# Performance work log

Measured on AMD Instinct MI355X. Metric: run time of the kernel, lower is better.

Reference implementation:

```python
import jax, jax.numpy as jnp
import numpy as np

B, N, D, H = 4, 2048, 1024, 16
HD = D // H
SCALE = D ** -0.5  # NOTE: original scales by dimension**-0.5 (not head_dim**-0.5)


def setup_inputs() -> dict:
    key = jax.random.key(0)
    k1, k2, k3 = jax.random.split(key, 3)
    x = jax.random.normal(k1, (B, N, D), dtype=jnp.float32)
    w_qkv = jax.random.normal(k2, (D, 3 * D), dtype=jnp.float32) * (D ** -0.5)
    w_proj = jax.random.normal(k3, (D, D), dtype=jnp.float32) * (D ** -0.5)
    b_proj = jnp.zeros((D,), dtype=jnp.float32)
    return {"x": x, "w_qkv": w_qkv, "w_proj": w_proj, "b_proj": b_proj}


def reference(x, w_qkv, w_proj, b_proj):
    # qkv projection: [B,N,3D] -> split into q,k,v each [B,H,N,HD]
    qkv = x @ w_qkv
    qkv = qkv.reshape(B, N, 3, H, HD).transpose(2, 0, 3, 1, 4)  # [3,B,H,N,HD]
    q, k, v = qkv[0], qkv[1], qkv[2]
    scores = jnp.einsum('bhid,bhjd->bhij', q, k) * SCALE
    attn = jax.nn.softmax(scores, axis=-1)
    out = jnp.einsum('bhij,bhjd->bhid', attn, v)  # [B,H,N,HD]
    out = out.transpose(0, 2, 1, 3).reshape(B, N, D)
    return out @ w_proj + b_proj
```

## Files before the change

kernel.cpp:

```cpp
#include <hip/hip_runtime.h>
#include <stdint.h>

#define Bdim 4
#define Nseq 2048
#define Dmod 1024
#define Hn   16
#define HD   64
#define SCALE 0.03125f
#define L2E   1.44269504089f

typedef __attribute__((ext_vector_type(8))) short short8;
typedef __attribute__((ext_vector_type(8))) unsigned short ushort8;
typedef __attribute__((ext_vector_type(4))) float f32x4;
typedef __attribute__((ext_vector_type(16))) float f32x16;

typedef __attribute__((address_space(3))) uint32_t lds_u32;
typedef __attribute__((address_space(1))) const uint32_t glob_u32;

static __device__ __forceinline__ void gload_lds16(const unsigned short* g, unsigned short* l) {
    __builtin_amdgcn_global_load_lds((glob_u32*)(const void*)g, (lds_u32*)(void*)l, 16, 0, 0);
}

static __device__ __forceinline__ unsigned short f2bf(float f) {
    union { float f; uint32_t u; } v; v.f = f;
    uint32_t r = (v.u + 0x7FFFu + ((v.u >> 16) & 1u)) >> 16;
    return (unsigned short)r;
}

__global__ __launch_bounds__(256) void cast_x_kernel(const float* __restrict__ in,
                                                     unsigned short* __restrict__ out, int n4) {
    int i = blockIdx.x * blockDim.x + threadIdx.x;
    int stride = gridDim.x * blockDim.x;
    for (; i < n4; i += stride) {
        float4 v = reinterpret_cast<const float4*>(in)[i];
        ushort4 o;
        o.x = f2bf(v.x); o.y = f2bf(v.y); o.z = f2bf(v.z); o.w = f2bf(v.w);
        reinterpret_cast<ushort4*>(out)[i] = o;
    }
}

__global__ void transpose_cast_kernel(const float* __restrict__ in,
                                      unsigned short* __restrict__ out, int R, int C) {
    __shared__ unsigned short t[32][33];
    int c0 = blockIdx.x * 32, r0 = blockIdx.y * 32;
    int tx = threadIdx.x, ty = threadIdx.y;
#pragma unroll
    for (int i = 0; i < 4; ++i)
        t[ty + i*8][tx] = f2bf(in[(size_t)(r0 + ty + i*8) * C + c0 + tx]);
    __syncthreads();
#pragma unroll
    for (int i = 0; i < 4; ++i)
        out[(size_t)(c0 + ty + i*8) * R + r0 + tx] = t[tx][ty + i*8];
}

template<bool OUT_BF16, bool BIAS>
__global__ __launch_bounds__(256) void gemm_bt_kernel(const unsigned short* __restrict__ A,
                                                      const unsigned short* __restrict__ Bt,
                                                      void* __restrict__ Cv,
                                                      const float* __restrict__ bias,
                                                      int M, int N, int K) {
    __shared__ unsigned short Al[128 * 64];
    __shared__ unsigned short Bl[128 * 64];
    int tid = threadIdx.x;
    int lane = tid & 63, wv = tid >> 6;
    int wr = (wv >> 1) * 64, wc = (wv & 1) * 64;
    int lr = lane & 15, lg = lane >> 4, lk = lg * 8;
    int m0 = blockIdx.y * 128, n0 = blockIdx.x * 128;

    int srow = wv * 8 + (lane >> 3);
    int scol = (lane & 7) * 8;
    const unsigned short* ag = A  + (size_t)(m0 + srow) * K + scol;
    const unsigned short* bg = Bt + (size_t)(n0 + srow) * K + scol;
    unsigned short* la = Al + wv * 512;
    unsigned short* lb = Bl + wv * 512;

    f32x4 acc[4][4];
#pragma unroll
    for (int i = 0; i < 4; ++i)
#pragma unroll
        for (int j = 0; j < 4; ++j) acc[i][j] = (f32x4)0.f;

    for (int k0 = 0; k0 < K; k0 += 64) {
        __syncthreads();
#pragma unroll
        for (int i = 0; i < 4; ++i) {
            gload_lds16(ag + (size_t)i * 32 * K + k0, la + i * 2048);
            gload_lds16(bg + (size_t)i * 32 * K + k0, lb + i * 2048);
        }
        __syncthreads();
#pragma unroll
        for (int ks = 0; ks < 2; ++ks) {
            short8 a[4], b[4];
#pragma unroll
            for (int mi = 0; mi < 4; ++mi)
                a[mi] = *reinterpret_cast<const short8*>(Al + (wr + mi*16 + lr) * 64 + ks*32 + lk);
#pragma unroll
            for (int nj = 0; nj < 4; ++nj)
                b[nj] = *reinterpret_cast<const short8*>(Bl + (wc + nj*16 + lr) * 64 + ks*32 + lk);
#pragma unroll
            for (int mi = 0; mi < 4; ++mi)
#pragma unroll
                for (int nj = 0; nj < 4; ++nj)
                    acc[mi][nj] = __builtin_amdgcn_mfma_f32_16x16x32_bf16(a[mi], b[nj], acc[mi][nj], 0, 0, 0);
        }
    }
#pragma unroll
    for (int mi = 0; mi < 4; ++mi) {
#pragma unroll
        for (int nj = 0; nj < 4; ++nj) {
            int r = m0 + wr + mi*16 + lg*4;
            int c = n0 + wc + nj*16 + lr;
            float bv = BIAS ? bias[c] : 0.f;
#pragma unroll
            for (int i = 0; i < 4; ++i) {
                float v = acc[mi][nj][i] + bv;
                if (OUT_BF16)
                    reinterpret_cast<unsigned short*>(Cv)[(size_t)(r + i) * N + c] = f2bf(v);
                else
                    reinterpret_cast<float*>(Cv)[(size_t)(r + i) * N + c] = v;
            }
        }
    }
}

__global__ __launch_bounds__(256) void transpose_v_kernel(const unsigned short* __restrict__ qkv,
                                                          unsigned short* __restrict__ vT) {
    __shared__ unsigned short t[64][68];
    int bh = blockIdx.y, b = bh >> 4, h = bh & 15;
    int j0 = blockIdx.x * 64;
    int tid = threadIdx.x;
#pragma unroll
    for (int p = 0; p < 4; ++p) {
        int e = p * 256 + tid;
        int jj = e >> 4;
        int d4 = (e & 15) * 4;
        const unsigned short* src = qkv + (size_t)(b*Nseq + j0 + jj) * 3072 + 2048 + h*64 + d4;
        ushort4 v = *reinterpret_cast<const ushort4*>(src);
        *reinterpret_cast<ushort4*>(&t[jj][d4]) = v;
    }
    __syncthreads();
#pragma unroll
    for (int p = 0; p < 4; ++p) {
        int e = p * 256 + tid;
        int d = e >> 4;
        int j4 = (e & 15) * 4;
        ushort4 v;
        v.x = t[j4 + 0][d]; v.y = t[j4 + 1][d]; v.z = t[j4 + 2][d]; v.w = t[j4 + 3][d];
        *reinterpret_cast<ushort4*>(vT + ((size_t)bh * 64 + d) * Nseq + j0 + j4) = v;
    }
}

__global__ __launch_bounds__(256, 2) void attn_kernel(const unsigned short* __restrict__ qkv,
                                                      const unsigned short* __restrict__ vT,
                                                      unsigned short* __restrict__ attn_o) {
    __shared__ unsigned short Kl[64 * 64];
    __shared__ unsigned short Vl[64 * 64];
    __shared__ unsigned short Pl[4 * 64 * 64];

    int w = blockIdx.x;
    int lid = (w & 7) * 64 + (w >> 3);
    int bh = lid >> 3, qb = lid & 7;
    int b = bh >> 4, h = bh & 15;

    int tid = threadIdx.x, lane = tid & 63, wv = tid >> 6;
    int lr = lane & 31, hi = lane >> 5;
    int q0 = qb * 256 + wv * 64;

    short8 qfA[4], qfB[4];
    {
        const unsigned short* qrowA = qkv + (size_t)(b * Nseq + q0 + lr) * 3072 + h * 64 + hi * 8;
        const unsigned short* qrowB = qrowA + (size_t)32 * 3072;
#pragma unroll
        for (int ks = 0; ks < 4; ++ks) {
            qfA[ks] = *reinterpret_cast<const short8*>(qrowA + ks * 16);
            qfB[ks] = *reinterpret_cast<const short8*>(qrowB + ks * 16);
        }
    }

    float mrunA = -1e30f, lrunA = 0.f, mrunB = -1e30f, lrunB = 0.f;
    f32x16 oA0 = (f32x16)0.f, oA1 = (f32x16)0.f, oB0 = (f32x16)0.f, oB1 = (f32x16)0.f;

    int sr = tid >> 2;
    int sc = (tid & 3) * 32;
    const unsigned short* kg = qkv + (size_t)(b * Nseq + sr) * 3072 + 1024 + h * 64 + sc / 2;
    const unsigned short* vg = vT + ((size_t)(bh * 64 + sr)) * Nseq + sc / 2;
    int swz0 = sr * 128 + ((sc) ^ ((sr & 7) << 4));
    int swz1 = sr * 128 + ((sc + 16) ^ ((sr & 7) << 4));
    int rswz = (lr & 7) << 4;
    char* PlW = (char*)Pl + wv * 8192 + lr * 128;

    ushort8 k0r = *reinterpret_cast<const ushort8*>(kg);
    ushort8 k1r = *reinterpret_cast<const ushort8*>(kg + 8);
    ushort8 v0r = *reinterpret_cast<const ushort8*>(vg);
    ushort8 v1r = *reinterpret_cast<const ushort8*>(vg + 8);

    for (int jt = 0; jt < Nseq; jt += 64) {
        __syncthreads();
        *reinterpret_cast<ushort8*>((char*)Kl + swz0) = k0r;
        *reinterpret_cast<ushort8*>((char*)Kl + swz1) = k1r;
        *reinterpret_cast<ushort8*>((char*)Vl + swz0) = v0r;
        *reinterpret_cast<ushort8*>((char*)Vl + swz1) = v1r;
        int jn = jt + 64;
        if (jn < Nseq) {
            k0r = *reinterpret_cast<const ushort8*>(kg + (size_t)jn * 3072);
            k1r = *reinterpret_cast<const ushort8*>(kg + (size_t)jn * 3072 + 8);
            v0r = *reinterpret_cast<const ushort8*>(vg + jn);
            v1r = *reinterpret_cast<const ushort8*>(vg + jn + 8);
        }
        __syncthreads();

        f32x16 sA0 = (f32x16)0.f, sA1 = (f32x16)0.f, sB0 = (f32x16)0.f, sB1 = (f32x16)0.f;
        __builtin_amdgcn_s_setprio(1);
#pragma unroll
        for (int ks = 0; ks < 4; ++ks) {
            int cb = ks * 32 + hi * 16;
            short8 kf0 = *reinterpret_cast<const short8*>((char*)Kl + lr * 128 + (cb ^ rswz));
            short8 kf1 = *reinterpret_cast<const short8*>((char*)Kl + (lr + 32) * 128 + (cb ^ rswz));
            sA0 = __builtin_amdgcn_mfma_f32_32x32x16_bf16(kf0, qfA[ks], sA0, 0, 0, 0);
            sA1 = __builtin_amdgcn_mfma_f32_32x32x16_bf16(kf1, qfA[ks], sA1, 0, 0, 0);
            sB0 = __builtin_amdgcn_mfma_f32_32x32x16_bf16(kf0, qfB[ks], sB0, 0, 0, 0);
            sB1 = __builtin_amdgcn_mfma_f32_32x32x16_bf16(kf1, qfB[ks], sB1, 0, 0, 0);
        }
        __builtin_amdgcn_s_setprio(0);

        float tA[16], tB[16];
#pragma unroll
        for (int i = 0; i < 16; ++i) { tA[i] = fmaxf(sA0[i], sA1[i]); tB[i] = fmaxf(sB0[i], sB1[i]); }
#pragma unroll
        for (int st = 8; st > 0; st >>= 1)
#pragma unroll
            for (int i = 0; i < st; ++i) { tA[i] = fmaxf(tA[i], tA[i + st]); tB[i] = fmaxf(tB[i], tB[i + st]); }
        float mlocA = fmaxf(tA[0], __shfl_xor(tA[0], 32)) * SCALE;
        float mlocB = fmaxf(tB[0], __shfl_xor(tB[0], 32)) * SCALE;

        if (!__all((mlocA <= mrunA + 8.f) && (mlocB <= mrunB + 8.f))) {
            float mnA = fmaxf(mrunA, mlocA);
            float fA = __builtin_amdgcn_exp2f((mrunA - mnA) * L2E);
            float mnB = fmaxf(mrunB, mlocB);
            float fB = __builtin_amdgcn_exp2f((mrunB - mnB) * L2E);
            lrunA *= fA; lrunB *= fB; mrunA = mnA; mrunB = mnB;
#pragma unroll
            for (int i = 0; i < 16; ++i) {
                oA0[i] *= fA; oA1[i] *= fA; oB0[i] *= fB; oB1[i] *= fB;
            }
        }

        const float c1 = SCALE * L2E;
        float c0A = -mrunA * L2E, c0B = -mrunB * L2E;
        float pA0[16], pA1[16], pB0[16], pB1[16];
#pragma unroll
        for (int i = 0; i < 16; ++i) {
            pA0[i] = __builtin_amdgcn_exp2f(fmaf(sA0[i], c1, c0A));
            pA1[i] = __builtin_amdgcn_exp2f(fmaf(sA1[i], c1, c0A));
            pB0[i] = __builtin_amdgcn_exp2f(fmaf(sB0[i], c1, c0B));
            pB1[i] = __builtin_amdgcn_exp2f(fmaf(sB1[i], c1, c0B));
        }

        uint32_t WA[16], WB[16];
#pragma unroll
        for (int m = 0; m < 8; ++m) {
            asm("v_cvt_pk_bf16_f32 %0, %1, %2" : "=v"(WA[m])   : "v"(pA0[2*m]), "v"(pA0[2*m+1]));
            asm("v_cvt_pk_bf16_f32 %0, %1, %2" : "=v"(WA[8+m]) : "v"(pA1[2*m]), "v"(pA1[2*m+1]));
            asm("v_cvt_pk_bf16_f32 %0, %1, %2" : "=v"(WB[m])   : "v"(pB0[2*m]), "v"(pB0[2*m+1]));
            asm("v_cvt_pk_bf16_f32 %0, %1, %2" : "=v"(WB[8+m]) : "v"(pB1[2*m]), "v"(pB1[2*m+1]));
        }
#pragma unroll
        for (int tt = 0; tt < 8; ++tt) {
            uint64_t valA = (uint64_t)WA[2*tt] | ((uint64_t)WA[2*tt+1] << 32);
            uint64_t valB = (uint64_t)WB[2*tt] | ((uint64_t)WB[2*tt+1] << 32);
            int off = (16*tt + 8*hi) ^ rswz;
            *reinterpret_cast<uint64_t*>(PlW + off) = valA;
            *reinterpret_cast<uint64_t*>(PlW + 4096 + off) = valB;
        }

        float aA[16], aB[16];
#pragma unroll
        for (int i = 0; i < 16; ++i) { aA[i] = pA0[i] + pA1[i]; aB[i] = pB0[i] + pB1[i]; }
#pragma unroll
        for (int st = 8; st > 0; st >>= 1)
#pragma unroll
            for (int i = 0; i < st; ++i) { aA[i] += aA[i + st]; aB[i] += aB[i + st]; }
        lrunA += aA[0] + __shfl_xor(aA[0], 32);
        lrunB += aB[0] + __shfl_xor(aB[0], 32);

        __builtin_amdgcn_s_setprio(1);
#pragma unroll
        for (int ks4 = 0; ks4 < 4; ++ks4) {
            int cb = ks4 * 32 + hi * 16;
            short8 vf0 = *reinterpret_cast<const short8*>((char*)Vl + lr * 128 + (cb ^ rswz));
            short8 vf1 = *reinterpret_cast<const short8*>((char*)Vl + (lr + 32) * 128 + (cb ^ rswz));
            short8 pfA = *reinterpret_cast<const short8*>(PlW + (cb ^ rswz));
            short8 pfB = *reinterpret_cast<const short8*>(PlW + 4096 + (cb ^ rswz));
            oA0 = __builtin_amdgcn_mfma_f32_32x32x16_bf16(vf0, pfA, oA0, 0, 0, 0);
            oA1 = __builtin_amdgcn_mfma_f32_32x32x16_bf16(vf1, pfA, oA1, 0, 0, 0);
            oB0 = __builtin_amdgcn_mfma_f32_32x32x16_bf16(vf0, pfB, oB0, 0, 0, 0);
            oB1 = __builtin_amdgcn_mfma_f32_32x32x16_bf16(vf1, pfB, oB1, 0, 0, 0);
        }
        __builtin_amdgcn_s_setprio(0);
    }

    float invA = 1.f / lrunA, invB = 1.f / lrunB;
    unsigned short* orowA = attn_o + (size_t)(b * Nseq + q0 + lr) * Dmod + h * 64;
    unsigned short* orowB = attn_o + (size_t)(b * Nseq + q0 + 32 + lr) * Dmod + h * 64;
#pragma unroll
    for (int db = 0; db < 2; ++db)
#pragma unroll
        for (int g = 0; g < 4; ++g) {
            int d = db * 32 + 8 * g + 4 * hi;
            ushort4 o4;
            o4.x = f2bf((db ? oA1[4*g+0] : oA0[4*g+0]) * invA);
            o4.y = f2bf((db ? oA1[4*g+1] : oA0[4*g+1]) * invA);
            o4.z = f2bf((db ? oA1[4*g+2] : oA0[4*g+2]) * invA);
            o4.w = f2bf((db ? oA1[4*g+3] : oA0[4*g+3]) * invA);
            *reinterpret_cast<ushort4*>(orowA + d) = o4;
            o4.x = f2bf((db ? oB1[4*g+0] : oB0[4*g+0]) * invB);
            o4.y = f2bf((db ? oB1[4*g+1] : oB0[4*g+1]) * invB);
            o4.z = f2bf((db ? oB1[4*g+2] : oB0[4*g+2]) * invB);
            o4.w = f2bf((db ? oB1[4*g+3] : oB0[4*g+3]) * invB);
            *reinterpret_cast<ushort4*>(orowB + d) = o4;
        }
}

extern "C" void kernel_launch(void* const* d_in, const int* in_sizes, int n_in,
                              void* d_out, int out_size, void* d_ws, size_t ws_size,
                              hipStream_t stream) {
    const float* x      = (const float*)d_in[0];
    const float* w_qkv  = (const float*)d_in[1];
    const float* w_proj = (const float*)d_in[2];
    const float* b_proj = (const float*)d_in[3];
    float* out = (float*)d_out;
    char* ws = (char*)d_ws;

    unsigned short* qkv    = (unsigned short*)(ws);
    unsigned short* vT     = (unsigned short*)(ws + 50331648);
    unsigned short* xb     = (unsigned short*)(ws + 67108864);
    unsigned short* attn_o = xb;
    unsigned short* wqkvT  = (unsigned short*)(ws + 83886080);
    unsigned short* wprojT = (unsigned short*)(ws + 90177536);

    cast_x_kernel<<<2048, 256, 0, stream>>>(x, xb, (Bdim*Nseq*Dmod)/4);
    transpose_cast_kernel<<<dim3(3072/32, 1024/32), dim3(32, 8), 0, stream>>>(w_qkv, wqkvT, 1024, 3072);
    transpose_cast_kernel<<<dim3(1024/32, 1024/32), dim3(32, 8), 0, stream>>>(w_proj, wprojT, 1024, 1024);
    gemm_bt_kernel<true, false><<<dim3(3072/128, 8192/128), 256, 0, stream>>>(
        xb, wqkvT, qkv, nullptr, Bdim*Nseq, 3*Dmod, Dmod);
    transpose_v_kernel<<<dim3(Nseq/64, Bdim*Hn), 256, 0, stream>>>(qkv, vT);
    attn_kernel<<<512, 256, 0, stream>>>(qkv, vT, attn_o);
    gemm_bt_kernel<false, true><<<dim3(1024/128, 8192/128), 256, 0, stream>>>(
        attn_o, wprojT, out, b_proj, Bdim*Nseq, Dmod, Dmod);
}
```

Before: 224.5 us.

## Double-buffer K/V tiles in attention and swizzle GEMM block order

Measured after the change: 226.2 us. Within noise of the previous version (+0.7%).

```diff
diff --git a/kernel.cpp b/kernel.cpp
--- a/kernel.cpp
+++ b/kernel.cpp
@@ -65,7 +65,12 @@
     int lane = tid & 63, wv = tid >> 6;
     int wr = (wv >> 1) * 64, wc = (wv & 1) * 64;
     int lr = lane & 15, lg = lane >> 4, lk = lg * 8;
-    int m0 = blockIdx.y * 128, n0 = blockIdx.x * 128;
+
+    int gx = gridDim.x;
+    int lin = blockIdx.y * gx + blockIdx.x;
+    int cpx = (gx * gridDim.y) >> 3;
+    int nl = (lin & 7) * cpx + (lin >> 3);
+    int m0 = (nl / gx) * 128, n0 = (nl % gx) * 128;
 
     int srow = wv * 8 + (lane >> 3);
     int scol = (lane & 7) * 8;
@@ -153,8 +158,8 @@
 __global__ __launch_bounds__(256, 2) void attn_kernel(const unsigned short* __restrict__ qkv,
                                                       const unsigned short* __restrict__ vT,
                                                       unsigned short* __restrict__ attn_o) {
-    __shared__ unsigned short Kl[64 * 64];
-    __shared__ unsigned short Vl[64 * 64];
+    __shared__ unsigned short Kl[2 * 64 * 64];
+    __shared__ unsigned short Vl[2 * 64 * 64];
     __shared__ unsigned short Pl[4 * 64 * 64];
 
     int w = blockIdx.x;
@@ -189,39 +194,53 @@
     int rswz = (lr & 7) << 4;
     char* PlW = (char*)Pl + wv * 8192 + lr * 128;
 
-    ushort8 k0r = *reinterpret_cast<const ushort8*>(kg);
-    ushort8 k1r = *reinterpret_cast<const ushort8*>(kg + 8);
-    ushort8 v0r = *reinterpret_cast<const ushort8*>(vg);
-    ushort8 v1r = *reinterpret_cast<const ushort8*>(vg + 8);
-
-    for (int jt = 0; jt < Nseq; jt += 64) {
+    {
+        ushort8 a0 = *reinterpret_cast<const ushort8*>(kg);
+        ushort8 a1 = *reinterpret_cast<const ushort8*>(kg + 8);
+        ushort8 a2 = *reinterpret_cast<const ushort8*>(vg);
+        ushort8 a3 = *reinterpret_cast<const ushort8*>(vg + 8);
+        *reinterpret_cast<ushort8*>((char*)Kl + swz0) = a0;
+        *reinterpret_cast<ushort8*>((char*)Kl + swz1) = a1;
+        *reinterpret_cast<ushort8*>((char*)Vl + swz0) = a2;
+        *reinterpret_cast<ushort8*>((char*)Vl + swz1) = a3;
+    }
+    ushort8 k0r = *reinterpret_cast<const ushort8*>(kg + (size_t)64 * 3072);
+    ushort8 k1r = *reinterpret_cast<const ushort8*>(kg + (size_t)64 * 3072 + 8);
+    ushort8 v0r = *reinterpret_cast<const ushort8*>(vg + 64);
+    ushort8 v1r = *reinterpret_cast<const ushort8*>(vg + 72);
+
+    int cur = 0;
+    for (int jt = 0; jt < Nseq; jt += 64, cur ^= 1) {
         __syncthreads();
-        *reinterpret_cast<ushort8*>((char*)Kl + swz0) = k0r;
-        *reinterpret_cast<ushort8*>((char*)Kl + swz1) = k1r;
-        *reinterpret_cast<ushort8*>((char*)Vl + swz0) = v0r;
-        *reinterpret_cast<ushort8*>((char*)Vl + swz1) = v1r;
-        int jn = jt + 64;
-        if (jn < Nseq) {
-            k0r = *reinterpret_cast<const ushort8*>(kg + (size_t)jn * 3072);
-            k1r = *reinterpret_cast<const ushort8*>(kg + (size_t)jn * 3072 + 8);
-            v0r = *reinterpret_cast<const ushort8*>(vg + jn);
-            v1r = *reinterpret_cast<const ushort8*>(vg + jn + 8);
-        }
-        __syncthreads();
+        int rb = cur * 8192, wb = rb ^ 8192;
 
         f32x16 sA0 = (f32x16)0.f, sA1 = (f32x16)0.f, sB0 = (f32x16)0.f, sB1 = (f32x16)0.f;
         __builtin_amdgcn_s_setprio(1);
 #pragma unroll
         for (int ks = 0; ks < 4; ++ks) {
             int cb = ks * 32 + hi * 16;
-            short8 kf0 = *reinterpret_cast<const short8*>((char*)Kl + lr * 128 + (cb ^ rswz));
-            short8 kf1 = *reinterpret_cast<const short8*>((char*)Kl + (lr + 32) * 128 + (cb ^ rswz));
+            short8 kf0 = *reinterpret_cast<const short8*>((char*)Kl + rb + lr * 128 + (cb ^ rswz));
+            short8 kf1 = *reinterpret_cast<const short8*>((char*)Kl + rb + (lr + 32) * 128 + (cb ^ rswz));
             sA0 = __builtin_amdgcn_mfma_f32_32x32x16_bf16(kf0, qfA[ks], sA0, 0, 0, 0);
             sA1 = __builtin_amdgcn_mfma_f32_32x32x16_bf16(kf1, qfA[ks], sA1, 0, 0, 0);
             sB0 = __builtin_amdgcn_mfma_f32_32x32x16_bf16(kf0, qfB[ks], sB0, 0, 0, 0);
             sB1 = __builtin_amdgcn_mfma_f32_32x32x16_bf16(kf1, qfB[ks], sB1, 0, 0, 0);
         }
         __builtin_amdgcn_s_setprio(0);
+
+        if (jt + 64 < Nseq) {
+            *reinterpret_cast<ushort8*>((char*)Kl + wb + swz0) = k0r;
+            *reinterpret_cast<ushort8*>((char*)Kl + wb + swz1) = k1r;
+            *reinterpret_cast<ushort8*>((char*)Vl + wb + swz0) = v0r;
+            *reinterpret_cast<ushort8*>((char*)Vl + wb + swz1) = v1r;
+            int jn = jt + 128;
+            if (jn < Nseq) {
+                k0r = *reinterpret_cast<const ushort8*>(kg + (size_t)jn * 3072);
+                k1r = *reinterpret_cast<const ushort8*>(kg + (size_t)jn * 3072 + 8);
+                v0r = *reinterpret_cast<const ushort8*>(vg + jn);
+                v1r = *reinterpret_cast<const ushort8*>(vg + jn + 8);
+            }
+        }
 
         float tA[16], tB[16];
 #pragma unroll
@@ -287,8 +306,8 @@
 #pragma unroll
         for (int ks4 = 0; ks4 < 4; ++ks4) {
             int cb = ks4 * 32 + hi * 16;
-            short8 vf0 = *reinterpret_cast<const short8*>((char*)Vl + lr * 128 + (cb ^ rswz));
-            short8 vf1 = *reinterpret_cast<const short8*>((char*)Vl + (lr + 32) * 128 + (cb ^ rswz));
+            short8 vf0 = *reinterpret_cast<const short8*>((char*)Vl + rb + lr * 128 + (cb ^ rswz));
+            short8 vf1 = *reinterpret_cast<const short8*>((char*)Vl + rb + (lr + 32) * 128 + (cb ^ rswz));
             short8 pfA = *reinterpret_cast<const short8*>(PlW + (cb ^ rswz));
             short8 pfB = *reinterpret_cast<const short8*>(PlW + 4096 + (cb ^ rswz));
             oA0 = __builtin_amdgcn_mfma_f32_32x32x16_bf16(vf0, pfA, oA0, 0, 0, 0);
```
